# Optimization experiments

Hardware: AMD Instinct MI355X
Metric: run time of the kernel (lower is better)

## Reference

```python
import jax, jax.numpy as jnp
import numpy as np

B, S, IN, E, H, NL = 64, 512, 1024, 128, 8, 4
D = E // H  # head dim = 16


def setup_inputs() -> dict:
    key = jax.random.key(0)
    ks = jax.random.split(key, 12)
    rn = lambda k, shape: jax.random.normal(k, shape, jnp.float32) * 0.02
    x = jax.random.normal(ks[0], (B, S, IN), jnp.float32)
    # per-recording valid lengths; recording 0 full-length so no attention key row is all-masked
    lengths = jax.random.randint(ks[1], (B,), 1, S + 1).at[0].set(S)
    key_padding_mask = jnp.arange(S)[None, :] >= lengths[:, None]  # (B,S) True = pad
    return {
        'x': x,
        'key_padding_mask': key_padding_mask,
        'embed_w': rn(ks[2], (IN, E)), 'embed_b': jnp.zeros((E,), jnp.float32),
        'qkv_w': rn(ks[3], (NL, 3, E, E)), 'qkv_b': jnp.zeros((NL, 3, E), jnp.float32),
        'out_w': rn(ks[4], (NL, E, E)), 'out_b': jnp.zeros((NL, E), jnp.float32),
        'ln_g': jnp.ones((NL, E), jnp.float32), 'ln_b': jnp.zeros((NL, E), jnp.float32),
        'ff1_w': rn(ks[5], (NL, E, 4 * E)), 'ff1_b': jnp.zeros((NL, 4 * E), jnp.float32),
        'ff2_w': rn(ks[6], (NL, 4 * E, E)), 'ff2_b': jnp.zeros((NL, E), jnp.float32),
        'fc1_w': rn(ks[7], (E, 32)), 'fc1_b': jnp.zeros((32,), jnp.float32),
        'fc2_w': rn(ks[8], (32, 1)), 'fc2_b': jnp.zeros((1,), jnp.float32),
    }


def _ln(x, g, b):
    m = x.mean(-1, keepdims=True)
    v = x.var(-1, keepdims=True)
    return (x - m) / jnp.sqrt(v + 1e-5) * g + b


def _pos_enc(s, e):
    pos = jnp.arange(s, dtype=jnp.float32)[:, None]
    i = jnp.arange(e)[None, :]
    angle = pos / jnp.power(jnp.float32(10000.0), (2 * (i // 2)).astype(jnp.float32) / e)
    return jnp.where(i % 2 == 0, jnp.sin(angle), jnp.cos(angle))  # (S,E)


def reference(x, key_padding_mask, embed_w, embed_b, qkv_w, qkv_b, out_w, out_b,
              ln_g, ln_b, ff1_w, ff1_b, ff2_w, ff2_b, fc1_w, fc1_b, fc2_w, fc2_b):
    h = x @ embed_w + embed_b  # (B,S,E)
    pe = _pos_enc(S, E)
    scale = 1.0 / jnp.sqrt(jnp.float32(D))
    # module uses batch_first=False MHA on (B,S,E): attention runs across recordings.
    # key_padding_mask.T -> (S,B): masked keys are recordings, per epoch position.
    keymask = key_padding_mask.T[:, None, None, :]  # (S,1,1,B)
    for l in range(NL):
        h = h + pe[None]  # pos enc re-added every block (as in source)
        res = h
        q = (h @ qkv_w[l, 0] + qkv_b[l, 0]).reshape(B, S, H, D)
        k = (h @ qkv_w[l, 1] + qkv_b[l, 1]).reshape(B, S, H, D)
        v = (h @ qkv_w[l, 2] + qkv_b[l, 2]).reshape(B, S, H, D)
        scores = jnp.einsum('ishd,jshd->shij', q, k) * scale  # (S,H,B,B)
        scores = jnp.where(keymask, -jnp.inf, scores)
        attn = jax.nn.softmax(scores, axis=-1)
        o = jnp.einsum('shij,jshd->ishd', attn, v).reshape(B, S, E)
        o = o @ out_w[l] + out_b[l]
        h = _ln(o + res, ln_g[l], ln_b[l])
        res = h
        ffo = jax.nn.relu(h @ ff1_w[l] + ff1_b[l]) @ ff2_w[l] + ff2_b[l]
        h = _ln(ffo + res, ln_g[l], ln_b[l])  # same LN params reused, as in source
    # masked mean pool over epochs (vectorized replacement of the python loop)
    valid = (~key_padding_mask).astype(h.dtype)  # (B,S)
    mean = jnp.einsum('bse,bs->be', h, valid) / valid.sum(axis=1)[:, None]
    out = jax.nn.relu(mean @ fc1_w + fc1_b) @ fc2_w + fc2_b  # (B,1)
    return jax.nn.sigmoid(out)
```

## Files before the change

kernel.cpp:

```cpp
#include <hip/hip_runtime.h>

#define Bb 64
#define Ss 512
#define INn 1024
#define Ee 128
#define Hh 8
#define Dd 16
#define NLl 4

typedef unsigned short u16;
typedef __attribute__((ext_vector_type(8))) short short8;
typedef __attribute__((ext_vector_type(4))) float f32x4;

__device__ __forceinline__ float b2f(unsigned u) { return __uint_as_float(u << 16); }
__device__ __forceinline__ u16 f2b(float f) {
    unsigned u = __float_as_uint(f);
    unsigned r = u + 0x7FFFu + ((u >> 16) & 1u);
    return (u16)(r >> 16);
}
__device__ __forceinline__ void up8(uint4 u, float* f) {
    f[0] = b2f(u.x & 0xffffu); f[1] = b2f(u.x >> 16);
    f[2] = b2f(u.y & 0xffffu); f[3] = b2f(u.y >> 16);
    f[4] = b2f(u.z & 0xffffu); f[5] = b2f(u.z >> 16);
    f[6] = b2f(u.w & 0xffffu); f[7] = b2f(u.w >> 16);
}
__device__ __forceinline__ uint2 pk4(float4 f) {
    uint2 r;
    r.x = (unsigned)f2b(f.x) | ((unsigned)f2b(f.y) << 16);
    r.y = (unsigned)f2b(f.z) | ((unsigned)f2b(f.w) << 16);
    return r;
}

#define GLOAD_LDS16(g, l) __builtin_amdgcn_global_load_lds( \
    (const __attribute__((address_space(1))) void*)(g),     \
    (__attribute__((address_space(3))) void*)(l), 16, 0, 0)

__global__ __launch_bounds__(256) void detect_kernel(const unsigned char* __restrict__ m,
                                                     int* __restrict__ flags) {
    int idx = blockIdx.x * 256 + threadIdx.x;
    int l0 = 0, l1 = 0, l23 = 0;
    for (int rep = 0; rep < 16; ++rep) {
        int i = idx * 16 + rep;
        if (m[i]) { int md = i & 3; if (md == 0) l0 = 1; else if (md == 1) l1 = 1; else l23 = 1; }
    }
    if (l0) atomicOr(&flags[0], 1);
    if (l1) atomicOr(&flags[1], 1);
    if (l23) atomicOr(&flags[2], 1);
}

__global__ __launch_bounds__(64) void lengths_kernel(const unsigned char* __restrict__ m,
                                                     const int* __restrict__ flags,
                                                     int* __restrict__ lengths) {
    int b = blockIdx.x, t = threadIdx.x;
    int enc = flags[1] ? 1 : (flags[2] ? 2 : 0);
    int cnt = 0;
    for (int s = t; s < Ss; s += 64) {
        int idx = b * Ss + s;
        int mm;
        if (enc == 1)      mm = (m[idx] != 0);
        else if (enc == 2) mm = (((const float*)(const void*)m)[idx] != 0.0f);
        else               mm = (((const int*)(const void*)m)[idx] != 0);
        cnt += (mm == 0);
    }
    cnt += __shfl_xor(cnt, 1);  cnt += __shfl_xor(cnt, 2);  cnt += __shfl_xor(cnt, 4);
    cnt += __shfl_xor(cnt, 8);  cnt += __shfl_xor(cnt, 16); cnt += __shfl_xor(cnt, 32);
    if (t == 0) lengths[b] = cnt;
}

__global__ __launch_bounds__(256) void pe_kernel(float* __restrict__ pe) {
    int idx = blockIdx.x * 256 + threadIdx.x;
    if (idx >= Ss * Ee) return;
    int s = idx >> 7, e = idx & 127;
    float expo = (float)(2 * (e >> 1)) * (1.0f / 128.0f);
    float freq = powf(10000.0f, -expo);
    float angle = (float)s * freq;
    pe[idx] = (e & 1) ? cosf(angle) : sinf(angle);
}

__global__ __launch_bounds__(256) void wprep_kernel(const float* __restrict__ ew,
                                                    const float* __restrict__ qw,
                                                    const float* __restrict__ ow,
                                                    const float* __restrict__ f1w,
                                                    const float* __restrict__ f2w,
                                                    u16* __restrict__ we, u16* __restrict__ wq,
                                                    u16* __restrict__ wo, u16* __restrict__ wf1,
                                                    u16* __restrict__ wf2) {
    int bid = blockIdx.x;
    const float* src; u16* dst; int K, N, tile;
    if (bid < 32)       { src = ew;  dst = we;  K = 1024; N = 128; tile = bid; }
    else if (bid < 80)  { int b = bid - 32;  int mat = b >> 2; src = qw  + (size_t)mat * 16384; dst = wq  + (size_t)mat * 16384; K = 128; N = 128; tile = b & 3; }
    else if (bid < 96)  { int b = bid - 80;  int mat = b >> 2; src = ow  + (size_t)mat * 16384; dst = wo  + (size_t)mat * 16384; K = 128; N = 128; tile = b & 3; }
    else if (bid < 160) { int b = bid - 96;  int mat = b >> 4; src = f1w + (size_t)mat * 65536; dst = wf1 + (size_t)mat * 65536; K = 128; N = 512; tile = b & 15; }
    else                { int b = bid - 160; int mat = b >> 4; src = f2w + (size_t)mat * 65536; dst = wf2 + (size_t)mat * 65536; K = 512; N = 128; tile = b & 15; }
    int ktiles = K >> 6;
    int k0 = (tile % ktiles) * 64, n0 = (tile / ktiles) * 64;
    __shared__ __align__(16) u16 t_s[64 * 68];
    int r = threadIdx.x >> 2, cq = (threadIdx.x & 3) * 16;
    const float* sp = src + (size_t)(k0 + r) * N + n0 + cq;
#pragma unroll
    for (int i = 0; i < 4; ++i) {
        float4 f = *(const float4*)(sp + 4 * i);
        *(uint2*)&t_s[r * 68 + cq + 4 * i] = pk4(f);
    }
    __syncthreads();
    u16 tmp[16];
#pragma unroll
    for (int kk = 0; kk < 16; ++kk) tmp[kk] = t_s[(cq + kk) * 68 + r];
    u16* dp = dst + (size_t)(n0 + r) * K + k0 + cq;
    *(uint4*)dp       = ((uint4*)tmp)[0];
    *(uint4*)(dp + 8) = ((uint4*)tmp)[1];
}

__global__ __launch_bounds__(256) void embed_gemm(const float* __restrict__ X,
                                                  const u16* __restrict__ Wt,
                                                  const float* __restrict__ bias,
                                                  const float* __restrict__ pe,
                                                  u16* __restrict__ C) {
    __shared__ __align__(16) u16 Af[64 * 68];
    __shared__ __align__(16) u16 Bs[128 * 64];
    const int tid = threadIdx.x;
    const int w = tid >> 6, lane = tid & 63, l16 = lane & 15, lhi = lane >> 4;
    const int row0 = blockIdx.x * 64;
    f32x4 acc[8];
#pragma unroll
    for (int ni = 0; ni < 8; ++ni) acc[ni] = (f32x4){0.f, 0.f, 0.f, 0.f};

    const int ar = tid >> 2, ak = (tid & 3) * 16;
    const int crow = tid >> 3, cc8 = (tid & 7) * 8;
    const int wave_lds = w * 512;
    const u16* Bbase = Wt + cc8;
    const float* Arow = X + (size_t)(row0 + ar) * 1024 + ak;

    for (int k0 = 0; k0 < 1024; k0 += 64) {
        __syncthreads();
#pragma unroll
        for (int i = 0; i < 4; ++i)
            GLOAD_LDS16(Bbase + (size_t)(i * 32 + crow) * 1024 + k0, &Bs[i * 2048 + wave_lds]);
#pragma unroll
        for (int i = 0; i < 4; ++i) {
            float4 f = *(const float4*)(Arow + k0 + 4 * i);
            *(uint2*)&Af[ar * 68 + ak + 4 * i] = pk4(f);
        }
        __syncthreads();
#pragma unroll
        for (int ks = 0; ks < 2; ++ks) {
            short8 af;
            ((uint2*)&af)[0] = *(const uint2*)&Af[(w * 16 + l16) * 68 + ks * 32 + lhi * 8];
            ((uint2*)&af)[1] = *(const uint2*)&Af[(w * 16 + l16) * 68 + ks * 32 + lhi * 8 + 4];
#pragma unroll
            for (int ni = 0; ni < 8; ++ni) {
                short8 bfr = *(const short8*)&Bs[(ni * 16 + l16) * 64 + ks * 32 + lhi * 8];
                acc[ni] = __builtin_amdgcn_mfma_f32_16x16x32_bf16(af, bfr, acc[ni], 0, 0, 0);
            }
        }
    }
    float biasr[8];
#pragma unroll
    for (int ni = 0; ni < 8; ++ni) biasr[ni] = bias[ni * 16 + l16];
#pragma unroll
    for (int reg = 0; reg < 4; ++reg) {
        int r = row0 + w * 16 + lhi * 4 + reg;
        const float* per = pe + (size_t)(r & 511) * 128;
        u16* crw = C + (size_t)r * 128;
#pragma unroll
        for (int ni = 0; ni < 8; ++ni) {
            int c = ni * 16 + l16;
            crw[c] = f2b(acc[ni][reg] + biasr[ni] + per[c]);
        }
    }
}

__global__ __launch_bounds__(256) void qkv_gemm(const u16* __restrict__ A,
                                                const u16* __restrict__ Wt,
                                                const float* __restrict__ bias,
                                                u16* __restrict__ Cq,
                                                u16* __restrict__ Ckv) {
    __shared__ __align__(16) u16 As[128 * 128];
    __shared__ __align__(16) u16 Bs[128 * 128];
    const int tid = threadIdx.x, w = tid >> 6, lane = tid & 63;
    const int l16 = lane & 15, lhi = lane >> 4;
    const int row0 = blockIdx.x * 128, col0 = blockIdx.y * 128;
    const int so = w * 512 + lane * 8;
#pragma unroll
    for (int i = 0; i < 8; ++i) {
        GLOAD_LDS16(A + (size_t)row0 * 128 + i * 2048 + so, &As[i * 2048 + w * 512]);
        GLOAD_LDS16(Wt + (size_t)col0 * 128 + i * 2048 + so, &Bs[i * 2048 + w * 512]);
    }
    __syncthreads();
    f32x4 acc[2][8];
#pragma unroll
    for (int mi = 0; mi < 2; ++mi)
#pragma unroll
        for (int ni = 0; ni < 8; ++ni) acc[mi][ni] = (f32x4){0.f, 0.f, 0.f, 0.f};
#pragma unroll
    for (int ks = 0; ks < 4; ++ks) {
        short8 af[2], bfr[8];
#pragma unroll
        for (int mi = 0; mi < 2; ++mi)
            af[mi] = *(const short8*)&As[(w * 32 + mi * 16 + l16) * 128 + ks * 32 + lhi * 8];
#pragma unroll
        for (int ni = 0; ni < 8; ++ni)
            bfr[ni] = *(const short8*)&Bs[(ni * 16 + l16) * 128 + ks * 32 + lhi * 8];
#pragma unroll
        for (int mi = 0; mi < 2; ++mi)
#pragma unroll
            for (int ni = 0; ni < 8; ++ni)
                acc[mi][ni] = __builtin_amdgcn_mfma_f32_16x16x32_bf16(af[mi], bfr[ni], acc[mi][ni], 0, 0, 0);
    }
    float biasr[8];
#pragma unroll
    for (int ni = 0; ni < 8; ++ni) biasr[ni] = bias[col0 + ni * 16 + l16];
#pragma unroll
    for (int mi = 0; mi < 2; ++mi)
#pragma unroll
        for (int reg = 0; reg < 4; ++reg) {
            int r = row0 + w * 32 + mi * 16 + lhi * 4 + reg;
            int orow = ((r & 511) << 6) + (r >> 9);
            u16* crw; int cbase;
            if (col0 == 0) { crw = Cq + (size_t)orow * 128; cbase = 0; }
            else           { crw = Ckv + (size_t)orow * 256; cbase = col0 - 128; }
#pragma unroll
            for (int ni = 0; ni < 8; ++ni)
                crw[cbase + ni * 16 + l16] = f2b(acc[mi][ni][reg] + biasr[ni]);
        }
}

__global__ __launch_bounds__(256) void attnout_kernel(const u16* __restrict__ qb,
                                                      const u16* __restrict__ kvb,
                                                      const u16* __restrict__ wo,
                                                      const float* __restrict__ outb,
                                                      const int* __restrict__ lengths,
                                                      const float* __restrict__ gamma,
                                                      const float* __restrict__ beta,
                                                      u16* __restrict__ h) {
    const int s = blockIdx.x;
    const int tid = threadIdx.x, w = tid >> 6, lane = tid & 63;
    const int l16 = lane & 15, lhi = lane >> 4;
    __shared__ __align__(16) u16 Vt[8 * 16 * 72];
    __shared__ __align__(16) u16 Ps[4 * 64 * 72];
    __shared__ __align__(16) u16 o_s[64 * 136];
    __shared__ int len_s[64];

    {
        int j = tid >> 2, c = tid & 3;
        const u16* src = kvb + ((size_t)(s * 64 + j)) * 256 + 128 + c * 32;
        u16 tmp[32];
        ((uint4*)tmp)[0] = *(const uint4*)src;
        ((uint4*)tmp)[1] = *(const uint4*)(src + 8);
        ((uint4*)tmp)[2] = *(const uint4*)(src + 16);
        ((uint4*)tmp)[3] = *(const uint4*)(src + 24);
#pragma unroll
        for (int e = 0; e < 32; ++e) {
            int hh = 2 * c + (e >> 4), d = e & 15;
            Vt[hh * 1152 + d * 72 + j] = tmp[e];
        }
    }
    if (tid < 64) len_s[tid] = lengths[tid];
    __syncthreads();

    bool mk[4];
#pragma unroll
    for (int jt = 0; jt < 4; ++jt) mk[jt] = (s >= len_s[jt * 16 + l16]);

    u16* pw = Ps + w * 4608;
#pragma unroll
    for (int hp = 0; hp < 2; ++hp) {
        const int hh = w * 2 + hp;
        short8 af[4];
#pragma unroll
        for (int it = 0; it < 4; ++it) {
            af[it] = (short8){0, 0, 0, 0, 0, 0, 0, 0};
            if (lhi < 2)
                af[it] = *(const short8*)(qb + ((size_t)(s * 64 + it * 16 + l16)) * 128 + hh * 16 + lhi * 8);
        }
        f32x4 sf[4][4];
#pragma unroll
        for (int jt = 0; jt < 4; ++jt) {
            short8 bf = (short8){0, 0, 0, 0, 0, 0, 0, 0};
            if (lhi < 2)
                bf = *(const short8*)(kvb + ((size_t)(s * 64 + jt * 16 + l16)) * 256 + hh * 16 + lhi * 8);
#pragma unroll
            for (int it = 0; it < 4; ++it)
                sf[it][jt] = __builtin_amdgcn_mfma_f32_16x16x32_bf16(af[it], bf, (f32x4){0.f, 0.f, 0.f, 0.f}, 0, 0, 0);
        }
        float inv[4][4];
#pragma unroll
        for (int it = 0; it < 4; ++it) {
#pragma unroll
            for (int reg = 0; reg < 4; ++reg) {
                float vv[4], mx = -1e30f;
#pragma unroll
                for (int jt = 0; jt < 4; ++jt) {
                    float xv = mk[jt] ? -1e30f : sf[it][jt][reg] * 0.25f;
                    vv[jt] = xv; mx = fmaxf(mx, xv);
                }
                mx = fmaxf(mx, __shfl_xor(mx, 1)); mx = fmaxf(mx, __shfl_xor(mx, 2));
                mx = fmaxf(mx, __shfl_xor(mx, 4)); mx = fmaxf(mx, __shfl_xor(mx, 8));
                float e4[4], sum = 0.f;
#pragma unroll
                for (int jt = 0; jt < 4; ++jt) {
                    float e = mk[jt] ? 0.f : __expf(vv[jt] - mx);
                    e4[jt] = e; sum += e;
                }
                sum += __shfl_xor(sum, 1); sum += __shfl_xor(sum, 2);
                sum += __shfl_xor(sum, 4); sum += __shfl_xor(sum, 8);
                inv[it][reg] = 1.0f / sum;
                int prow = it * 16 + lhi * 4 + reg;
#pragma unroll
                for (int jt = 0; jt < 4; ++jt)
                    pw[prow * 72 + jt * 16 + l16] = f2b(e4[jt]);
            }
        }
        f32x4 ao[4];
#pragma unroll
        for (int it = 0; it < 4; ++it) ao[it] = (f32x4){0.f, 0.f, 0.f, 0.f};
        short8 vb[2];
#pragma unroll
        for (int ksv = 0; ksv < 2; ++ksv)
            vb[ksv] = *(const short8*)&Vt[hh * 1152 + l16 * 72 + ksv * 32 + lhi * 8];
#pragma unroll
        for (int it = 0; it < 4; ++it)
#pragma unroll
            for (int ksv = 0; ksv < 2; ++ksv) {
                short8 pa = *(const short8*)&pw[(it * 16 + l16) * 72 + ksv * 32 + lhi * 8];
                ao[it] = __builtin_amdgcn_mfma_f32_16x16x32_bf16(pa, vb[ksv], ao[it], 0, 0, 0);
            }
#pragma unroll
        for (int it = 0; it < 4; ++it)
#pragma unroll
            for (int reg = 0; reg < 4; ++reg)
                o_s[(it * 16 + lhi * 4 + reg) * 136 + hh * 16 + l16] = f2b(ao[it][reg] * inv[it][reg]);
    }
    __syncthreads();

    f32x4 acc[8];
#pragma unroll
    for (int ni = 0; ni < 8; ++ni) acc[ni] = (f32x4){0.f, 0.f, 0.f, 0.f};
#pragma unroll
    for (int ks = 0; ks < 4; ++ks) {
        short8 af = *(const short8*)&o_s[(w * 16 + l16) * 136 + ks * 32 + lhi * 8];
#pragma unroll
        for (int ni = 0; ni < 8; ++ni) {
            short8 bf = *(const short8*)(wo + (size_t)(ni * 16 + l16) * 128 + ks * 32 + lhi * 8);
            acc[ni] = __builtin_amdgcn_mfma_f32_16x16x32_bf16(af, bf, acc[ni], 0, 0, 0);
        }
    }
    float biasr[8], gr[8], br[8];
#pragma unroll
    for (int ni = 0; ni < 8; ++ni) {
        int c = ni * 16 + l16;
        biasr[ni] = outb[c]; gr[ni] = gamma[c]; br[ni] = beta[c];
    }
#pragma unroll
    for (int reg = 0; reg < 4; ++reg) {
        int b = w * 16 + lhi * 4 + reg;
        size_t rbase = ((size_t)b * 512 + s) * 128;
        float v[8], sm = 0.f, s2 = 0.f;
#pragma unroll
        for (int ni = 0; ni < 8; ++ni) {
            float x = acc[ni][reg] + biasr[ni] + b2f(h[rbase + ni * 16 + l16]);
            v[ni] = x; sm += x; s2 += x * x;
        }
        sm += __shfl_xor(sm, 1); sm += __shfl_xor(sm, 2);
        sm += __shfl_xor(sm, 4); sm += __shfl_xor(sm, 8);
        s2 += __shfl_xor(s2, 1); s2 += __shfl_xor(s2, 2);
        s2 += __shfl_xor(s2, 4); s2 += __shfl_xor(s2, 8);
        float mean = sm * (1.0f / 128.0f);
        float var = s2 * (1.0f / 128.0f) - mean * mean;
        float rstd = rsqrtf(fmaxf(var, 0.0f) + 1e-5f);
#pragma unroll
        for (int ni = 0; ni < 8; ++ni)
            h[rbase + ni * 16 + l16] = f2b((v[ni] - mean) * rstd * gr[ni] + br[ni]);
    }
}

__global__ __launch_bounds__(256) void ff_fused(const u16* __restrict__ hbuf,
                                                const u16* __restrict__ w1t,
                                                const u16* __restrict__ w2t,
                                                const float* __restrict__ b1,
                                                const float* __restrict__ b2,
                                                const float* __restrict__ gamma,
                                                const float* __restrict__ beta,
                                                const float* __restrict__ pe,
                                                u16* __restrict__ hout) {
    __shared__ __align__(16) u16 A_s[16384];
    __shared__ __align__(16) u16 W1_s[16384];
    __shared__ __align__(16) u16 W2_s[16384];
    __shared__ __align__(16) u16 T_s[16384];
    const int tid = threadIdx.x, w = tid >> 6, lane = tid & 63;
    const int l16 = lane & 15, lhi = lane >> 4;
    const int row0 = blockIdx.x * 128;
    const int so = w * 512 + lane * 8;
#pragma unroll
    for (int i = 0; i < 8; ++i)
        GLOAD_LDS16(hbuf + (size_t)row0 * 128 + i * 2048 + so, &A_s[i * 2048 + w * 512]);

    f32x4 acc2[2][8];
#pragma unroll
    for (int mi = 0; mi < 2; ++mi)
#pragma unroll
        for (int ni = 0; ni < 8; ++ni) acc2[mi][ni] = (f32x4){0.f, 0.f, 0.f, 0.f};

    for (int nc = 0; nc < 4; ++nc) {
        __syncthreads();
#pragma unroll
        for (int i = 0; i < 8; ++i) {
            GLOAD_LDS16(w1t + nc * 16384 + i * 2048 + so, &W1_s[i * 2048 + w * 512]);
            int slot = i * 2048 + so;
            GLOAD_LDS16(w2t + (size_t)(slot >> 7) * 512 + nc * 128 + (slot & 127),
                        &W2_s[i * 2048 + w * 512]);
        }
        __syncthreads();
        f32x4 acc1[2][8];
#pragma unroll
        for (int mi = 0; mi < 2; ++mi)
#pragma unroll
            for (int ni = 0; ni < 8; ++ni) acc1[mi][ni] = (f32x4){0.f, 0.f, 0.f, 0.f};
#pragma unroll
        for (int ks = 0; ks < 4; ++ks) {
            short8 af[2], bfr[8];
#pragma unroll
            for (int mi = 0; mi < 2; ++mi)
                af[mi] = *(const short8*)&A_s[(w * 32 + mi * 16 + l16) * 128 + ks * 32 + lhi * 8];
#pragma unroll
            for (int ni = 0; ni < 8; ++ni)
                bfr[ni] = *(const short8*)&W1_s[(ni * 16 + l16) * 128 + ks * 32 + lhi * 8];
#pragma unroll
            for (int mi = 0; mi < 2; ++mi)
#pragma unroll
                for (int ni = 0; ni < 8; ++ni)
                    acc1[mi][ni] = __builtin_amdgcn_mfma_f32_16x16x32_bf16(af[mi], bfr[ni], acc1[mi][ni], 0, 0, 0);
        }
        float bb[8];
#pragma unroll
        for (int ni = 0; ni < 8; ++ni) bb[ni] = b1[nc * 128 + ni * 16 + l16];
#pragma unroll
        for (int mi = 0; mi < 2; ++mi)
#pragma unroll
            for (int reg = 0; reg < 4; ++reg)
#pragma unroll
                for (int ni = 0; ni < 8; ++ni)
                    T_s[(w * 32 + mi * 16 + lhi * 4 + reg) * 128 + ni * 16 + l16] =
                        f2b(fmaxf(acc1[mi][ni][reg] + bb[ni], 0.0f));
#pragma unroll
        for (int ks = 0; ks < 4; ++ks) {
            short8 pa[2], bfr[8];
#pragma unroll
            for (int mi = 0; mi < 2; ++mi)
                pa[mi] = *(const short8*)&T_s[(w * 32 + mi * 16 + l16) * 128 + ks * 32 + lhi * 8];
#pragma unroll
            for (int ni = 0; ni < 8; ++ni)
                bfr[ni] = *(const short8*)&W2_s[(ni * 16 + l16) * 128 + ks * 32 + lhi * 8];
#pragma unroll
            for (int mi = 0; mi < 2; ++mi)
#pragma unroll
                for (int ni = 0; ni < 8; ++ni)
                    acc2[mi][ni] = __builtin_amdgcn_mfma_f32_16x16x32_bf16(pa[mi], bfr[ni], acc2[mi][ni], 0, 0, 0);
        }
    }
    float b2r[8], gr[8], br[8];
#pragma unroll
    for (int ni = 0; ni < 8; ++ni) {
        int c = ni * 16 + l16;
        b2r[ni] = b2[c]; gr[ni] = gamma[c]; br[ni] = beta[c];
    }
#pragma unroll
    for (int mi = 0; mi < 2; ++mi)
#pragma unroll
        for (int reg = 0; reg < 4; ++reg) {
            int lrow = w * 32 + mi * 16 + lhi * 4 + reg;
            int r = row0 + lrow;
            float v[8], sm = 0.f, s2 = 0.f;
#pragma unroll
            for (int ni = 0; ni < 8; ++ni) {
                float x = acc2[mi][ni][reg] + b2r[ni] + b2f(A_s[lrow * 128 + ni * 16 + l16]);
                v[ni] = x; sm += x; s2 += x * x;
            }
            sm += __shfl_xor(sm, 1); sm += __shfl_xor(sm, 2);
            sm += __shfl_xor(sm, 4); sm += __shfl_xor(sm, 8);
            s2 += __shfl_xor(s2, 1); s2 += __shfl_xor(s2, 2);
            s2 += __shfl_xor(s2, 4); s2 += __shfl_xor(s2, 8);
            float mean = sm * (1.0f / 128.0f);
            float var = s2 * (1.0f / 128.0f) - mean * mean;
            float rstd = rsqrtf(fmaxf(var, 0.0f) + 1e-5f);
            u16* crw = hout + (size_t)r * 128;
#pragma unroll
            for (int ni = 0; ni < 8; ++ni) {
                int c = ni * 16 + l16;
                float val = (v[ni] - mean) * rstd * gr[ni] + br[ni];
                if (pe) val += pe[(size_t)(r & 511) * 128 + c];
                crw[c] = f2b(val);
            }
        }
}

__global__ __launch_bounds__(256) void pool_kernel(const u16* __restrict__ h,
                                                   const int* __restrict__ lengths,
                                                   float* __restrict__ meanp) {
    int b = blockIdx.x, e = threadIdx.x & 127, q = threadIdx.x >> 7;
    int len = lengths[b];
    float s = 0.0f;
    for (int t = q; t < len; t += 2) s += b2f(h[((size_t)b * Ss + t) * Ee + e]);
    __shared__ float red[256];
    red[threadIdx.x] = s;
    __syncthreads();
    if (threadIdx.x < 128)
        meanp[b * Ee + threadIdx.x] = (red[threadIdx.x] + red[threadIdx.x + 128]) / (float)len;
}

__global__ __launch_bounds__(64) void head_kernel(const float* __restrict__ meanp,
                                                  const float* __restrict__ fc1w,
                                                  const float* __restrict__ fc1b,
                                                  const float* __restrict__ fc2w,
                                                  const float* __restrict__ fc2b,
                                                  float* __restrict__ out) {
    int b = blockIdx.x, j = threadIdx.x;
    __shared__ float z[32];
    if (j < 32) {
        float a = fc1b[j];
        for (int e = 0; e < 128; ++e) a = fmaf(meanp[b * 128 + e], fc1w[e * 32 + j], a);
        z[j] = fmaxf(a, 0.0f);
    }
    __syncthreads();
    if (j == 0) {
        float a = fc2b[0];
#pragma unroll
        for (int t = 0; t < 32; ++t) a = fmaf(z[t], fc2w[t], a);
        out[b] = 1.0f / (1.0f + expf(-a));
    }
}

extern "C" void kernel_launch(void* const* d_in, const int* in_sizes, int n_in,
                              void* d_out, int out_size, void* d_ws, size_t ws_size,
                              hipStream_t stream) {
    (void)in_sizes; (void)n_in; (void)out_size; (void)ws_size;
    const float* x        = (const float*)d_in[0];
    const unsigned char* mask = (const unsigned char*)d_in[1];
    const float* embed_w  = (const float*)d_in[2];
    const float* embed_b  = (const float*)d_in[3];
    const float* qkv_w    = (const float*)d_in[4];
    const float* qkv_b    = (const float*)d_in[5];
    const float* out_w    = (const float*)d_in[6];
    const float* out_b    = (const float*)d_in[7];
    const float* ln_g     = (const float*)d_in[8];
    const float* ln_b     = (const float*)d_in[9];
    const float* ff1_w    = (const float*)d_in[10];
    const float* ff1_b    = (const float*)d_in[11];
    const float* ff2_w    = (const float*)d_in[12];
    const float* ff2_b    = (const float*)d_in[13];
    const float* fc1_w    = (const float*)d_in[14];
    const float* fc1_b    = (const float*)d_in[15];
    const float* fc2_w    = (const float*)d_in[16];
    const float* fc2_b    = (const float*)d_in[17];

    char* wsb = (char*)d_ws;
    int*   lengths = (int*)wsb;
    int*   flags   = (int*)(wsb + 256);
    float* pe      = (float*)(wsb + 512);
    u16* wt_embed  = (u16*)(wsb + 262656);
    u16* wt_qkv    = (u16*)(wsb + 524800);
    u16* wt_out    = (u16*)(wsb + 918016);
    u16* wt_ff1    = (u16*)(wsb + 1049088);
    u16* wt_ff2    = (u16*)(wsb + 1573376);
    u16* hbuf      = (u16*)(wsb + 2097664);
    u16* qb        = (u16*)(wsb + 10486272);
    u16* kvb       = (u16*)(wsb + 18874880);
    float* meanp   = (float*)(wsb + 35652096);

    hipMemsetAsync(flags, 0, 12, stream);
    detect_kernel<<<8, 256, 0, stream>>>(mask, flags);
    lengths_kernel<<<64, 64, 0, stream>>>(mask, flags, lengths);
    pe_kernel<<<256, 256, 0, stream>>>(pe);
    wprep_kernel<<<224, 256, 0, stream>>>(embed_w, qkv_w, out_w, ff1_w, ff2_w,
                                          wt_embed, wt_qkv, wt_out, wt_ff1, wt_ff2);

    embed_gemm<<<512, 256, 0, stream>>>(x, wt_embed, embed_b, pe, hbuf);

    for (int l = 0; l < NLl; ++l) {
        qkv_gemm<<<dim3(256, 3), 256, 0, stream>>>(
            hbuf, wt_qkv + (size_t)l * 49152, qkv_b + l * 384, qb, kvb);
        attnout_kernel<<<512, 256, 0, stream>>>(
            qb, kvb, wt_out + (size_t)l * 16384, out_b + l * 128,
            lengths, ln_g + l * 128, ln_b + l * 128, hbuf);
        ff_fused<<<256, 256, 0, stream>>>(
            hbuf, wt_ff1 + (size_t)l * 65536, wt_ff2 + (size_t)l * 65536,
            ff1_b + l * 512, ff2_b + l * 128,
            ln_g + l * 128, ln_b + l * 128, (l < 3) ? pe : nullptr, hbuf);
    }

    pool_kernel<<<64, 256, 0, stream>>>(hbuf, lengths, meanp);
    head_kernel<<<64, 64, 0, stream>>>(meanp, fc1_w, fc1_b, fc2_w, fc2_b, (float*)d_out);
}
```

Measured before the change: 446.2 us.

## Switch hidden state to seq-major layout, merge prep kernels, shrink FF tile

Merges the mask detection, length counting, positional-encoding and weight-prep kernels into one launch, and merges pooling with the head MLP. Stores the hidden state in (S,B) row order so the qkv and attention kernels no longer scatter rows. The qkv GEMM now reads weight fragments directly from global memory instead of staging them in LDS. The fused FF kernel uses 64-row tiles with a single shared weight buffer, doubling the grid and cutting LDS use, at the cost of extra syncs and serialised W1/W2 loads.

```diff
diff --git a/kernel.cpp b/kernel.cpp
--- a/kernel.cpp
+++ b/kernel.cpp
@@ -35,67 +35,69 @@
     (const __attribute__((address_space(1))) void*)(g),     \
     (__attribute__((address_space(3))) void*)(l), 16, 0, 0)
 
-__global__ __launch_bounds__(256) void detect_kernel(const unsigned char* __restrict__ m,
-                                                     int* __restrict__ flags) {
-    int idx = blockIdx.x * 256 + threadIdx.x;
-    int l0 = 0, l1 = 0, l23 = 0;
-    for (int rep = 0; rep < 16; ++rep) {
-        int i = idx * 16 + rep;
-        if (m[i]) { int md = i & 3; if (md == 0) l0 = 1; else if (md == 1) l1 = 1; else l23 = 1; }
-    }
-    if (l0) atomicOr(&flags[0], 1);
-    if (l1) atomicOr(&flags[1], 1);
-    if (l23) atomicOr(&flags[2], 1);
-}
-
-__global__ __launch_bounds__(64) void lengths_kernel(const unsigned char* __restrict__ m,
-                                                     const int* __restrict__ flags,
-                                                     int* __restrict__ lengths) {
-    int b = blockIdx.x, t = threadIdx.x;
-    int enc = flags[1] ? 1 : (flags[2] ? 2 : 0);
-    int cnt = 0;
-    for (int s = t; s < Ss; s += 64) {
-        int idx = b * Ss + s;
-        int mm;
-        if (enc == 1)      mm = (m[idx] != 0);
-        else if (enc == 2) mm = (((const float*)(const void*)m)[idx] != 0.0f);
-        else               mm = (((const int*)(const void*)m)[idx] != 0);
-        cnt += (mm == 0);
-    }
-    cnt += __shfl_xor(cnt, 1);  cnt += __shfl_xor(cnt, 2);  cnt += __shfl_xor(cnt, 4);
-    cnt += __shfl_xor(cnt, 8);  cnt += __shfl_xor(cnt, 16); cnt += __shfl_xor(cnt, 32);
-    if (t == 0) lengths[b] = cnt;
-}
-
-__global__ __launch_bounds__(256) void pe_kernel(float* __restrict__ pe) {
-    int idx = blockIdx.x * 256 + threadIdx.x;
-    if (idx >= Ss * Ee) return;
-    int s = idx >> 7, e = idx & 127;
-    float expo = (float)(2 * (e >> 1)) * (1.0f / 128.0f);
-    float freq = powf(10000.0f, -expo);
-    float angle = (float)s * freq;
-    pe[idx] = (e & 1) ? cosf(angle) : sinf(angle);
-}
-
-__global__ __launch_bounds__(256) void wprep_kernel(const float* __restrict__ ew,
-                                                    const float* __restrict__ qw,
-                                                    const float* __restrict__ ow,
-                                                    const float* __restrict__ f1w,
-                                                    const float* __restrict__ f2w,
-                                                    u16* __restrict__ we, u16* __restrict__ wq,
-                                                    u16* __restrict__ wo, u16* __restrict__ wf1,
-                                                    u16* __restrict__ wf2) {
-    int bid = blockIdx.x;
+__global__ __launch_bounds__(256) void prep_kernel(const unsigned char* __restrict__ m,
+                                                   int* __restrict__ lengths,
+                                                   float* __restrict__ pe,
+                                                   const float* __restrict__ ew,
+                                                   const float* __restrict__ qw,
+                                                   const float* __restrict__ ow,
+                                                   const float* __restrict__ f1w,
+                                                   const float* __restrict__ f2w,
+                                                   u16* __restrict__ we, u16* __restrict__ wq,
+                                                   u16* __restrict__ wo, u16* __restrict__ wf1,
+                                                   u16* __restrict__ wf2) {
+    const int bid = blockIdx.x, tid = threadIdx.x;
+    if (bid == 0) {
+        __shared__ int lf[3];
+        __shared__ int part[256];
+        if (tid < 3) lf[tid] = 0;
+        __syncthreads();
+        int l0 = 0, l1 = 0, l23 = 0;
+        for (int i = tid * 128; i < tid * 128 + 128; ++i) {
+            if (m[i]) { int md = i & 3; if (md == 0) l0 = 1; else if (md == 1) l1 = 1; else l23 = 1; }
+        }
+        if (l0) atomicOr(&lf[0], 1);
+        if (l1) atomicOr(&lf[1], 1);
+        if (l23) atomicOr(&lf[2], 1);
+        __syncthreads();
+        int enc = lf[1] ? 1 : (lf[2] ? 2 : 0);
+        int b = tid >> 2, q = tid & 3, cnt = 0;
+        for (int s = q * 128; s < q * 128 + 128; ++s) {
+            int idx = b * Ss + s;
+            int mm;
+            if (enc == 1)      mm = (m[idx] != 0);
+            else if (enc == 2) mm = (((const float*)(const void*)m)[idx] != 0.0f);
+            else               mm = (((const int*)(const void*)m)[idx] != 0);
+            cnt += (mm == 0);
+        }
+        part[tid] = cnt;
+        __syncthreads();
+        if (tid < 64)
+            lengths[tid] = part[tid * 4] + part[tid * 4 + 1] + part[tid * 4 + 2] + part[tid * 4 + 3];
+        return;
+    }
+    if (bid <= 2) {
+        for (int i = tid; i < 32768; i += 256) {
+            int idx = (bid - 1) * 32768 + i;
+            int s = idx >> 7, e = idx & 127;
+            float expo = (float)(2 * (e >> 1)) * (1.0f / 128.0f);
+            float freq = powf(10000.0f, -expo);
+            float angle = (float)s * freq;
+            pe[idx] = (e & 1) ? cosf(angle) : sinf(angle);
+        }
+        return;
+    }
+    int tb = bid - 3;
     const float* src; u16* dst; int K, N, tile;
-    if (bid < 32)       { src = ew;  dst = we;  K = 1024; N = 128; tile = bid; }
-    else if (bid < 80)  { int b = bid - 32;  int mat = b >> 2; src = qw  + (size_t)mat * 16384; dst = wq  + (size_t)mat * 16384; K = 128; N = 128; tile = b & 3; }
-    else if (bid < 96)  { int b = bid - 80;  int mat = b >> 2; src = ow  + (size_t)mat * 16384; dst = wo  + (size_t)mat * 16384; K = 128; N = 128; tile = b & 3; }
-    else if (bid < 160) { int b = bid - 96;  int mat = b >> 4; src = f1w + (size_t)mat * 65536; dst = wf1 + (size_t)mat * 65536; K = 128; N = 512; tile = b & 15; }
-    else                { int b = bid - 160; int mat = b >> 4; src = f2w + (size_t)mat * 65536; dst = wf2 + (size_t)mat * 65536; K = 512; N = 128; tile = b & 15; }
+    if (tb < 32)       { src = ew;  dst = we;  K = 1024; N = 128; tile = tb; }
+    else if (tb < 80)  { int b = tb - 32;  int mat = b >> 2; src = qw  + (size_t)mat * 16384; dst = wq  + (size_t)mat * 16384; K = 128; N = 128; tile = b & 3; }
+    else if (tb < 96)  { int b = tb - 80;  int mat = b >> 2; src = ow  + (size_t)mat * 16384; dst = wo  + (size_t)mat * 16384; K = 128; N = 128; tile = b & 3; }
+    else if (tb < 160) { int b = tb - 96;  int mat = b >> 4; src = f1w + (size_t)mat * 65536; dst = wf1 + (size_t)mat * 65536; K = 128; N = 512; tile = b & 15; }
+    else               { int b = tb - 160; int mat = b >> 4; src = f2w + (size_t)mat * 65536; dst = wf2 + (size_t)mat * 65536; K = 512; N = 128; tile = b & 15; }
     int ktiles = K >> 6;
     int k0 = (tile % ktiles) * 64, n0 = (tile / ktiles) * 64;
     __shared__ __align__(16) u16 t_s[64 * 68];
-    int r = threadIdx.x >> 2, cq = (threadIdx.x & 3) * 16;
+    int r = tid >> 2, cq = (tid & 3) * 16;
     const float* sp = src + (size_t)(k0 + r) * N + n0 + cq;
 #pragma unroll
     for (int i = 0; i < 4; ++i) {
@@ -160,8 +162,10 @@
 #pragma unroll
     for (int reg = 0; reg < 4; ++reg) {
         int r = row0 + w * 16 + lhi * 4 + reg;
-        const float* per = pe + (size_t)(r & 511) * 128;
-        u16* crw = C + (size_t)r * 128;
+        int s = r & 511;
+        int orow = s * 64 + (r >> 9);
+        const float* per = pe + (size_t)s * 128;
+        u16* crw = C + (size_t)orow * 128;
 #pragma unroll
         for (int ni = 0; ni < 8; ++ni) {
             int c = ni * 16 + l16;
@@ -176,16 +180,13 @@
                                                 u16* __restrict__ Cq,
                                                 u16* __restrict__ Ckv) {
     __shared__ __align__(16) u16 As[128 * 128];
-    __shared__ __align__(16) u16 Bs[128 * 128];
     const int tid = threadIdx.x, w = tid >> 6, lane = tid & 63;
     const int l16 = lane & 15, lhi = lane >> 4;
     const int row0 = blockIdx.x * 128, col0 = blockIdx.y * 128;
     const int so = w * 512 + lane * 8;
 #pragma unroll
-    for (int i = 0; i < 8; ++i) {
+    for (int i = 0; i < 8; ++i)
         GLOAD_LDS16(A + (size_t)row0 * 128 + i * 2048 + so, &As[i * 2048 + w * 512]);
-        GLOAD_LDS16(Wt + (size_t)col0 * 128 + i * 2048 + so, &Bs[i * 2048 + w * 512]);
-    }
     __syncthreads();
     f32x4 acc[2][8];
 #pragma unroll
@@ -200,7 +201,7 @@
             af[mi] = *(const short8*)&As[(w * 32 + mi * 16 + l16) * 128 + ks * 32 + lhi * 8];
 #pragma unroll
         for (int ni = 0; ni < 8; ++ni)
-            bfr[ni] = *(const short8*)&Bs[(ni * 16 + l16) * 128 + ks * 32 + lhi * 8];
+            bfr[ni] = *(const short8*)(Wt + (size_t)(col0 + ni * 16 + l16) * 128 + ks * 32 + lhi * 8);
 #pragma unroll
         for (int mi = 0; mi < 2; ++mi)
 #pragma unroll
@@ -215,10 +216,9 @@
 #pragma unroll
         for (int reg = 0; reg < 4; ++reg) {
             int r = row0 + w * 32 + mi * 16 + lhi * 4 + reg;
-            int orow = ((r & 511) << 6) + (r >> 9);
             u16* crw; int cbase;
-            if (col0 == 0) { crw = Cq + (size_t)orow * 128; cbase = 0; }
-            else           { crw = Ckv + (size_t)orow * 256; cbase = col0 - 128; }
+            if (col0 == 0) { crw = Cq + (size_t)r * 128; cbase = 0; }
+            else           { crw = Ckv + (size_t)r * 256; cbase = col0 - 128; }
 #pragma unroll
             for (int ni = 0; ni < 8; ++ni)
                 crw[cbase + ni * 16 + l16] = f2b(acc[mi][ni][reg] + biasr[ni]);
@@ -353,8 +353,8 @@
     }
 #pragma unroll
     for (int reg = 0; reg < 4; ++reg) {
-        int b = w * 16 + lhi * 4 + reg;
-        size_t rbase = ((size_t)b * 512 + s) * 128;
+        int row = w * 16 + lhi * 4 + reg;
+        size_t rbase = ((size_t)(s * 64 + row)) * 128;
         float v[8], sm = 0.f, s2 = 0.f;
 #pragma unroll
         for (int ni = 0; ni < 8; ++ni) {
@@ -383,79 +383,64 @@
                                                 const float* __restrict__ beta,
                                                 const float* __restrict__ pe,
                                                 u16* __restrict__ hout) {
-    __shared__ __align__(16) u16 A_s[16384];
-    __shared__ __align__(16) u16 W1_s[16384];
-    __shared__ __align__(16) u16 W2_s[16384];
-    __shared__ __align__(16) u16 T_s[16384];
+    __shared__ __align__(16) u16 A_s[64 * 128];
+    __shared__ __align__(16) u16 T_s[64 * 128];
+    __shared__ __align__(16) u16 W_s[128 * 128];
     const int tid = threadIdx.x, w = tid >> 6, lane = tid & 63;
     const int l16 = lane & 15, lhi = lane >> 4;
-    const int row0 = blockIdx.x * 128;
+    const int row0 = blockIdx.x * 64;
     const int so = w * 512 + lane * 8;
 #pragma unroll
-    for (int i = 0; i < 8; ++i)
+    for (int i = 0; i < 4; ++i)
         GLOAD_LDS16(hbuf + (size_t)row0 * 128 + i * 2048 + so, &A_s[i * 2048 + w * 512]);
 
-    f32x4 acc2[2][8];
-#pragma unroll
-    for (int mi = 0; mi < 2; ++mi)
-#pragma unroll
-        for (int ni = 0; ni < 8; ++ni) acc2[mi][ni] = (f32x4){0.f, 0.f, 0.f, 0.f};
+    f32x4 acc2[8];
+#pragma unroll
+    for (int ni = 0; ni < 8; ++ni) acc2[ni] = (f32x4){0.f, 0.f, 0.f, 0.f};
 
     for (int nc = 0; nc < 4; ++nc) {
         __syncthreads();
 #pragma unroll
+        for (int i = 0; i < 8; ++i)
+            GLOAD_LDS16(w1t + nc * 16384 + i * 2048 + so, &W_s[i * 2048 + w * 512]);
+        __syncthreads();
+        f32x4 acc1[8];
+#pragma unroll
+        for (int ni = 0; ni < 8; ++ni) acc1[ni] = (f32x4){0.f, 0.f, 0.f, 0.f};
+#pragma unroll
+        for (int ks = 0; ks < 4; ++ks) {
+            short8 af = *(const short8*)&A_s[(w * 16 + l16) * 128 + ks * 32 + lhi * 8];
+#pragma unroll
+            for (int ni = 0; ni < 8; ++ni) {
+                short8 bfr = *(const short8*)&W_s[(ni * 16 + l16) * 128 + ks * 32 + lhi * 8];
+                acc1[ni] = __builtin_amdgcn_mfma_f32_16x16x32_bf16(af, bfr, acc1[ni], 0, 0, 0);
+            }
+        }
+        float bb[8];
+#pragma unroll
+        for (int ni = 0; ni < 8; ++ni) bb[ni] = b1[nc * 128 + ni * 16 + l16];
+#pragma unroll
+        for (int reg = 0; reg < 4; ++reg)
+#pragma unroll
+            for (int ni = 0; ni < 8; ++ni)
+                T_s[(w * 16 + lhi * 4 + reg) * 128 + ni * 16 + l16] =
+                    f2b(fmaxf(acc1[ni][reg] + bb[ni], 0.0f));
+        __syncthreads();
+#pragma unroll
         for (int i = 0; i < 8; ++i) {
-            GLOAD_LDS16(w1t + nc * 16384 + i * 2048 + so, &W1_s[i * 2048 + w * 512]);
             int slot = i * 2048 + so;
             GLOAD_LDS16(w2t + (size_t)(slot >> 7) * 512 + nc * 128 + (slot & 127),
-                        &W2_s[i * 2048 + w * 512]);
-        }
-        __syncthreads();
-        f32x4 acc1[2][8];
-#pragma unroll
-        for (int mi = 0; mi < 2; ++mi)
-#pragma unroll
-            for (int ni = 0; ni < 8; ++ni) acc1[mi][ni] = (f32x4){0.f, 0.f, 0.f, 0.f};
+                        &W_s[i * 2048 + w * 512]);
+        }
+        __syncthreads();
 #pragma unroll
         for (int ks = 0; ks < 4; ++ks) {
-            short8 af[2], bfr[8];
-#pragma unroll
-            for (int mi = 0; mi < 2; ++mi)
-                af[mi] = *(const short8*)&A_s[(w * 32 + mi * 16 + l16) * 128 + ks * 32 + lhi * 8];
-#pragma unroll
-            for (int ni = 0; ni < 8; ++ni)
-                bfr[ni] = *(const short8*)&W1_s[(ni * 16 + l16) * 128 + ks * 32 + lhi * 8];
-#pragma unroll
-            for (int mi = 0; mi < 2; ++mi)
-#pragma unroll
-                for (int ni = 0; ni < 8; ++ni)
-                    acc1[mi][ni] = __builtin_amdgcn_mfma_f32_16x16x32_bf16(af[mi], bfr[ni], acc1[mi][ni], 0, 0, 0);
-        }
-        float bb[8];
-#pragma unroll
-        for (int ni = 0; ni < 8; ++ni) bb[ni] = b1[nc * 128 + ni * 16 + l16];
-#pragma unroll
-        for (int mi = 0; mi < 2; ++mi)
-#pragma unroll
-            for (int reg = 0; reg < 4; ++reg)
-#pragma unroll
-                for (int ni = 0; ni < 8; ++ni)
-                    T_s[(w * 32 + mi * 16 + lhi * 4 + reg) * 128 + ni * 16 + l16] =
-                        f2b(fmaxf(acc1[mi][ni][reg] + bb[ni], 0.0f));
-#pragma unroll
-        for (int ks = 0; ks < 4; ++ks) {
-            short8 pa[2], bfr[8];
-#pragma unroll
-            for (int mi = 0; mi < 2; ++mi)
-                pa[mi] = *(const short8*)&T_s[(w * 32 + mi * 16 + l16) * 128 + ks * 32 + lhi * 8];
-#pragma unroll
-            for (int ni = 0; ni < 8; ++ni)
-                bfr[ni] = *(const short8*)&W2_s[(ni * 16 + l16) * 128 + ks * 32 + lhi * 8];
-#pragma unroll
-            for (int mi = 0; mi < 2; ++mi)
-#pragma unroll
-                for (int ni = 0; ni < 8; ++ni)
-                    acc2[mi][ni] = __builtin_amdgcn_mfma_f32_16x16x32_bf16(pa[mi], bfr[ni], acc2[mi][ni], 0, 0, 0);
+            short8 pa = *(const short8*)&T_s[(w * 16 + l16) * 128 + ks * 32 + lhi * 8];
+#pragma unroll
+            for (int ni = 0; ni < 8; ++ni) {
+                short8 bfr = *(const short8*)&W_s[(ni * 16 + l16) * 128 + ks * 32 + lhi * 8];
+                acc2[ni] = __builtin_amdgcn_mfma_f32_16x16x32_bf16(pa, bfr, acc2[ni], 0, 0, 0);
+            }
         }
     }
     float b2r[8], gr[8], br[8];
@@ -465,64 +450,59 @@
         b2r[ni] = b2[c]; gr[ni] = gamma[c]; br[ni] = beta[c];
     }
 #pragma unroll
-    for (int mi = 0; mi < 2; ++mi)
-#pragma unroll
-        for (int reg = 0; reg < 4; ++reg) {
-            int lrow = w * 32 + mi * 16 + lhi * 4 + reg;
-            int r = row0 + lrow;
-            float v[8], sm = 0.f, s2 = 0.f;
-#pragma unroll
-            for (int ni = 0; ni < 8; ++ni) {
-                float x = acc2[mi][ni][reg] + b2r[ni] + b2f(A_s[lrow * 128 + ni * 16 + l16]);
-                v[ni] = x; sm += x; s2 += x * x;
-            }
-            sm += __shfl_xor(sm, 1); sm += __shfl_xor(sm, 2);
-            sm += __shfl_xor(sm, 4); sm += __shfl_xor(sm, 8);
-            s2 += __shfl_xor(s2, 1); s2 += __shfl_xor(s2, 2);
-            s2 += __shfl_xor(s2, 4); s2 += __shfl_xor(s2, 8);
-            float mean = sm * (1.0f / 128.0f);
-            float var = s2 * (1.0f / 128.0f) - mean * mean;
-            float rstd = rsqrtf(fmaxf(var, 0.0f) + 1e-5f);
-            u16* crw = hout + (size_t)r * 128;
-#pragma unroll
-            for (int ni = 0; ni < 8; ++ni) {
-                int c = ni * 16 + l16;
-                float val = (v[ni] - mean) * rstd * gr[ni] + br[ni];
-                if (pe) val += pe[(size_t)(r & 511) * 128 + c];
-                crw[c] = f2b(val);
-            }
-        }
-}
-
-__global__ __launch_bounds__(256) void pool_kernel(const u16* __restrict__ h,
-                                                   const int* __restrict__ lengths,
-                                                   float* __restrict__ meanp) {
-    int b = blockIdx.x, e = threadIdx.x & 127, q = threadIdx.x >> 7;
+    for (int reg = 0; reg < 4; ++reg) {
+        int lrow = w * 16 + lhi * 4 + reg;
+        int r = row0 + lrow;
+        float v[8], sm = 0.f, s2 = 0.f;
+#pragma unroll
+        for (int ni = 0; ni < 8; ++ni) {
+            float x = acc2[ni][reg] + b2r[ni] + b2f(A_s[lrow * 128 + ni * 16 + l16]);
+            v[ni] = x; sm += x; s2 += x * x;
+        }
+        sm += __shfl_xor(sm, 1); sm += __shfl_xor(sm, 2);
+        sm += __shfl_xor(sm, 4); sm += __shfl_xor(sm, 8);
+        s2 += __shfl_xor(s2, 1); s2 += __shfl_xor(s2, 2);
+        s2 += __shfl_xor(s2, 4); s2 += __shfl_xor(s2, 8);
+        float mean = sm * (1.0f / 128.0f);
+        float var = s2 * (1.0f / 128.0f) - mean * mean;
+        float rstd = rsqrtf(fmaxf(var, 0.0f) + 1e-5f);
+        u16* crw = hout + (size_t)r * 128;
+#pragma unroll
+        for (int ni = 0; ni < 8; ++ni) {
+            int c = ni * 16 + l16;
+            float val = (v[ni] - mean) * rstd * gr[ni] + br[ni];
+            if (pe) val += pe[(size_t)(r >> 6) * 128 + c];
+            crw[c] = f2b(val);
+        }
+    }
+}
+
+__global__ __launch_bounds__(256) void poolhead_kernel(const u16* __restrict__ h,
+                                                       const int* __restrict__ lengths,
+                                                       const float* __restrict__ fc1w,
+                                                       const float* __restrict__ fc1b,
+                                                       const float* __restrict__ fc2w,
+                                                       const float* __restrict__ fc2b,
+                                                       float* __restrict__ out) {
+    int b = blockIdx.x, tid = threadIdx.x;
+    int e = tid & 127, half = tid >> 7;
     int len = lengths[b];
     float s = 0.0f;
-    for (int t = q; t < len; t += 2) s += b2f(h[((size_t)b * Ss + t) * Ee + e]);
+    for (int t = half; t < len; t += 2) s += b2f(h[((size_t)(t * 64 + b)) * 128 + e]);
     __shared__ float red[256];
-    red[threadIdx.x] = s;
-    __syncthreads();
-    if (threadIdx.x < 128)
-        meanp[b * Ee + threadIdx.x] = (red[threadIdx.x] + red[threadIdx.x + 128]) / (float)len;
-}
-
-__global__ __launch_bounds__(64) void head_kernel(const float* __restrict__ meanp,
-                                                  const float* __restrict__ fc1w,
-                                                  const float* __restrict__ fc1b,
-                                                  const float* __restrict__ fc2w,
-                                                  const float* __restrict__ fc2b,
-                                                  float* __restrict__ out) {
-    int b = blockIdx.x, j = threadIdx.x;
+    __shared__ float mp[128];
     __shared__ float z[32];
-    if (j < 32) {
-        float a = fc1b[j];
-        for (int e = 0; e < 128; ++e) a = fmaf(meanp[b * 128 + e], fc1w[e * 32 + j], a);
-        z[j] = fmaxf(a, 0.0f);
-    }
-    __syncthreads();
-    if (j == 0) {
+    red[tid] = s;
+    __syncthreads();
+    if (tid < 128) mp[tid] = (red[tid] + red[tid + 128]) / (float)len;
+    __syncthreads();
+    if (tid < 32) {
+        float a = fc1b[tid];
+        for (int k = 0; k < 128; ++k) a = fmaf(mp[k], fc1w[k * 32 + tid], a);
+        z[tid] = fmaxf(a, 0.0f);
+    }
+    __syncthreads();
+    if (tid == 0) {
         float a = fc2b[0];
 #pragma unroll
         for (int t = 0; t < 32; ++t) a = fmaf(z[t], fc2w[t], a);
@@ -555,7 +535,6 @@
 
     char* wsb = (char*)d_ws;
     int*   lengths = (int*)wsb;
-    int*   flags   = (int*)(wsb + 256);
     float* pe      = (float*)(wsb + 512);
     u16* wt_embed  = (u16*)(wsb + 262656);
     u16* wt_qkv    = (u16*)(wsb + 524800);
@@ -565,14 +544,10 @@
     u16* hbuf      = (u16*)(wsb + 2097664);
     u16* qb        = (u16*)(wsb + 10486272);
     u16* kvb       = (u16*)(wsb + 18874880);
-    float* meanp   = (float*)(wsb + 35652096);
-
-    hipMemsetAsync(flags, 0, 12, stream);
-    detect_kernel<<<8, 256, 0, stream>>>(mask, flags);
-    lengths_kernel<<<64, 64, 0, stream>>>(mask, flags, lengths);
-    pe_kernel<<<256, 256, 0, stream>>>(pe);
-    wprep_kernel<<<224, 256, 0, stream>>>(embed_w, qkv_w, out_w, ff1_w, ff2_w,
-                                          wt_embed, wt_qkv, wt_out, wt_ff1, wt_ff2);
+
+    prep_kernel<<<227, 256, 0, stream>>>(mask, lengths, pe,
+                                         embed_w, qkv_w, out_w, ff1_w, ff2_w,
+                                         wt_embed, wt_qkv, wt_out, wt_ff1, wt_ff2);
 
     embed_gemm<<<512, 256, 0, stream>>>(x, wt_embed, embed_b, pe, hbuf);
 
@@ -582,12 +557,12 @@
         attnout_kernel<<<512, 256, 0, stream>>>(
             qb, kvb, wt_out + (size_t)l * 16384, out_b + l * 128,
             lengths, ln_g + l * 128, ln_b + l * 128, hbuf);
-        ff_fused<<<256, 256, 0, stream>>>(
+        ff_fused<<<512, 256, 0, stream>>>(
             hbuf, wt_ff1 + (size_t)l * 65536, wt_ff2 + (size_t)l * 65536,
             ff1_b + l * 512, ff2_b + l * 128,
             ln_g + l * 128, ln_b + l * 128, (l < 3) ? pe : nullptr, hbuf);
     }
 
-    pool_kernel<<<64, 256, 0, stream>>>(hbuf, lengths, meanp);
-    head_kernel<<<64, 64, 0, stream>>>(meanp, fc1_w, fc1_b, fc2_w, fc2_b, (float*)d_out);
-}
+    poolhead_kernel<<<64, 256, 0, stream>>>(hbuf, lengths, fc1_w, fc1_b, fc2_w, fc2_b,
+                                            (float*)d_out);
+}
```

Result: slower. 530.4 us (+18.9%).
